# Kernel optimization log

Measured on AMD Instinct MI355X. Metric: run time of the kernel, lower is better.

## Reference

```python
import jax, jax.numpy as jnp
import numpy as np

V = 100000   # vertices
C = 64       # in channels
D = 64       # out channels
W = 8        # weight matrices
DEG = 16     # neighbors per vertex
E = V * DEG  # edges


def setup_inputs() -> dict:
    key = jax.random.key(0)
    k = jax.random.split(key, 6)
    data = jax.random.normal(k[0], (V, C), dtype=jnp.float32)
    # fixed-degree adjacency: vertex i has DEG neighbors (arbitrary dst)
    edge_src = jnp.repeat(jnp.arange(V, dtype=jnp.int32), DEG)        # [E] sorted
    edge_dst = jax.random.randint(k[1], (E,), 0, V, dtype=jnp.int32)  # [E]
    edge_vals = jnp.full((E,), 1.0 / DEG, dtype=jnp.float32)          # row-normalized
    var_u = 0.1 * jax.random.normal(k[2], (C, W), dtype=jnp.float32)
    var_c = 0.1 * jax.random.normal(k[3], (W,), dtype=jnp.float32)
    var_w = 0.1 * jax.random.normal(k[4], (W, C, D), dtype=jnp.float32)
    var_b = 0.1 * jax.random.normal(k[5], (D,), dtype=jnp.float32)
    return {"data": data, "edge_src": edge_src, "edge_dst": edge_dst,
            "edge_vals": edge_vals, "var_u": var_u, "var_c": var_c,
            "var_w": var_w, "var_b": var_b}


def reference(data, edge_src, edge_dst, edge_vals, var_u, var_c, var_w, var_b):
    # translation_invariant=True => var_v = -var_u
    num_v = data.shape[0]
    x_u = data @ var_u            # [V, W]
    x_v = data @ (-var_u)         # [V, W]
    # edge logits and exp-normalize over the W weight matrices (softmax == exp/sum)
    logits = x_u[edge_src] + x_v[edge_dst] + var_c   # [E, W]
    q = jax.nn.softmax(logits, axis=-1)              # [E, W]
    # gathered neighbor features, pre-scaled by adjacency values
    x_sep = data[edge_dst] * edge_vals[:, None]      # [E, C]
    y = jnp.zeros((num_v, var_w.shape[-1]), dtype=data.dtype)
    for m in range(var_c.shape[0]):  # small fixed loop over W weight matrices
        agg = jax.ops.segment_sum(q[:, m:m + 1] * x_sep, edge_src,
                                  num_segments=num_v)  # [V, C]
        y = y + agg @ var_w[m]                          # [V, D]
    return y + var_b
```

## Files before the change

### kernel.cpp

```cpp
#include <hip/hip_runtime.h>

typedef _Float16 half2_t __attribute__((ext_vector_type(2)));
typedef _Float16 half4_t __attribute__((ext_vector_type(4)));
typedef _Float16 half8_t __attribute__((ext_vector_type(8)));
typedef __attribute__((ext_vector_type(4))) float f32x4;

#define NV 100000
#define NTILE 6250
#define GRID 512
#define LDSZ 81920

#define VMWAIT(N) asm volatile("s_waitcnt vmcnt(" #N ")" ::: "memory")
#define LGKM0     asm volatile("s_waitcnt lgkmcnt(0)" ::: "memory")
#define FENCE     asm volatile("" ::: "memory")

__device__ __forceinline__ unsigned cvt_pk_u(float a, float b) {
  auto h = __builtin_amdgcn_cvt_pkrtz(a, b);
  return __builtin_bit_cast(unsigned, h);
}
__device__ __forceinline__ half2_t u2h(unsigned u) { return __builtin_bit_cast(half2_t, u); }
__device__ __forceinline__ unsigned lds_off(const void* p) {
  return (unsigned)(size_t)(const __attribute__((address_space(3))) char*)p;
}
__device__ __forceinline__ void load16_to_lds(const void* g, void* s) {
  __builtin_amdgcn_global_load_lds(
      (const __attribute__((address_space(1))) unsigned int*)g,
      (__attribute__((address_space(3))) unsigned int*)s, 16, 0, 0);
}

__global__ __launch_bounds__(256) void k1_prep(const float* __restrict__ data,
                                               const float* __restrict__ var_u,
                                               const float* __restrict__ var_w,
                                               unsigned short* __restrict__ data_h,
                                               unsigned short* __restrict__ xu_h,
                                               unsigned short* __restrict__ Bt) {
  __shared__ float u_lds[512];
  int tid = threadIdx.x;
  if (blockIdx.x < 128) {
    int t = blockIdx.x * 256 + tid;
    int d = t >> 9, k = t & 511;
    _Float16 h = (_Float16)var_w[k * 64 + d];
    Bt[t] = __builtin_bit_cast(unsigned short, h);
  }
  u_lds[tid] = var_u[tid];
  u_lds[tid + 256] = var_u[tid + 256];
  __syncthreads();
  int v = blockIdx.x * 256 + tid;
  if (v >= NV) return;
  const float4* dp = (const float4*)(data + v * 64);
  float acc[8];
#pragma unroll
  for (int w = 0; w < 8; ++w) acc[w] = 0.f;
  uint4* ob = (uint4*)(data_h + v * 64);
#pragma unroll
  for (int q = 0; q < 8; ++q) {
    float4 a4 = dp[q * 2], b4 = dp[q * 2 + 1];
    int c0 = q * 8;
#pragma unroll
    for (int w = 0; w < 8; ++w)
      acc[w] += a4.x * u_lds[(c0 + 0) * 8 + w] + a4.y * u_lds[(c0 + 1) * 8 + w]
              + a4.z * u_lds[(c0 + 2) * 8 + w] + a4.w * u_lds[(c0 + 3) * 8 + w]
              + b4.x * u_lds[(c0 + 4) * 8 + w] + b4.y * u_lds[(c0 + 5) * 8 + w]
              + b4.z * u_lds[(c0 + 6) * 8 + w] + b4.w * u_lds[(c0 + 7) * 8 + w];
    uint4 pk;
    pk.x = cvt_pk_u(a4.x, a4.y); pk.y = cvt_pk_u(a4.z, a4.w);
    pk.z = cvt_pk_u(b4.x, b4.y); pk.w = cvt_pk_u(b4.z, b4.w);
    ob[q] = pk;
  }
  uint4 xp;
  xp.x = cvt_pk_u(acc[0], acc[1]); xp.y = cvt_pk_u(acc[2], acc[3]);
  xp.z = cvt_pk_u(acc[4], acc[5]); xp.w = cvt_pk_u(acc[6], acc[7]);
  *(uint4*)(xu_h + v * 8) = xp;
}

#define PREPASS(XUDs, LINs, XS)                                               \
  {                                                                           \
    uint4 xd4 = *(const uint4*)((XUDs) + (wave * 64 + l) * 16);               \
    float evv = ((const float*)((LINs) + 1024))[wave * 64 + l];               \
    half2_t xm01 = u2h((XS).x), xm23 = u2h((XS).y);                           \
    half2_t xm45 = u2h((XS).z), xm67 = u2h((XS).w);                           \
    half2_t xd01 = u2h(xd4.x), xd23 = u2h(xd4.y);                             \
    half2_t xd45 = u2h(xd4.z), xd67 = u2h(xd4.w);                             \
    float ex0 = __expf((float)xm01[0] - (float)xd01[0] + c8[0]);              \
    float ex1 = __expf((float)xm01[1] - (float)xd01[1] + c8[1]);              \
    float ex2 = __expf((float)xm23[0] - (float)xd23[0] + c8[2]);              \
    float ex3 = __expf((float)xm23[1] - (float)xd23[1] + c8[3]);              \
    float ex4 = __expf((float)xm45[0] - (float)xd45[0] + c8[4]);              \
    float ex5 = __expf((float)xm45[1] - (float)xd45[1] + c8[5]);              \
    float ex6 = __expf((float)xm67[0] - (float)xd67[0] + c8[6]);              \
    float ex7 = __expf((float)xm67[1] - (float)xd67[1] + c8[7]);              \
    float ssum = ((ex0 + ex1) + (ex2 + ex3)) + ((ex4 + ex5) + (ex6 + ex7));   \
    float rs = __builtin_amdgcn_rcpf(ssum) * evv;                             \
    uint4 qq;                                                                 \
    qq.x = cvt_pk_u(ex0 * rs, ex1 * rs);                                      \
    qq.y = cvt_pk_u(ex2 * rs, ex3 * rs);                                      \
    qq.z = cvt_pk_u(ex4 * rs, ex5 * rs);                                      \
    qq.w = cvt_pk_u(ex6 * rs, ex7 * rs);                                      \
    int vv = l >> 4, jq = (l >> 2) & 3, jl = l & 3;                           \
    char* qb = (XUDs) + wave * 1024 + vv * 256;                               \
    _Pragma("unroll")                                                         \
    for (int m = 0; m < 8; ++m) {                                             \
      unsigned short hv = (unsigned short)((&qq.x)[m >> 1] >> ((m & 1) * 16));\
      int byte = (((m ^ vv) & 7) << 5) + (((jq ^ vv ^ m) & 3) << 3) + jl * 2; \
      *(unsigned short*)(qb + byte) = hv;                                     \
    }                                                                         \
  }

__global__ __launch_bounds__(256, 2) void k2_main(
    const unsigned short* __restrict__ data_h,
    const unsigned short* __restrict__ xu_h,
    const int* __restrict__ edge_dst,
    const float* __restrict__ edge_vals,
    const unsigned short* __restrict__ Bt,
    const float* __restrict__ var_c,
    const float* __restrict__ var_b,
    float* __restrict__ y) {
  extern __shared__ __align__(16) char smem[];
  char* XB0  = smem;
  char* XUD0 = smem + 65536;
  char* LIN0 = smem + 73728;

  int tid = threadIdx.x;
  int wave = tid >> 6;
  int l = tid & 63;
  int q4 = l >> 4;
  int row = l & 15;
  int col = row + wave * 16;

  uint4 btf[16];
#pragma unroll
  for (int ks = 0; ks < 16; ++ks)
    btf[ks] = *(const uint4*)(Bt + (col * 512 + ks * 32 + q4 * 8));
  float c8[8];
#pragma unroll
  for (int m = 0; m < 8; ++m) c8[m] = var_c[m];
  float bias = var_b[col];

#define LIN_DMA(SL, TS)                                                        \
  { char* lb_ = LIN0 + (SL) * 2048;                                            \
    if ((wave & 1) == 0)                                                       \
      load16_to_lds(edge_dst + (size_t)(TS) * 256 + l * 4, lb_);               \
    else                                                                       \
      load16_to_lds(edge_vals + (size_t)(TS) * 256 + l * 4, lb_ + 1024); }
#define XUD_DMA(SL, LSL)                                                       \
  { const int* ld_ = (const int*)(LIN0 + (LSL) * 2048);                        \
    int dv_ = ld_[wave * 64 + l];                                              \
    load16_to_lds(xu_h + (size_t)dv_ * 8, XUD0 + (SL) * 4096 + wave * 1024); }
#define X_DMA(SL, LSL)                                                         \
  { const int* ld_ = (const int*)(LIN0 + (LSL) * 2048);                        \
    int j_ = ((l >> 3) & 3) * 4 + ((l >> 1) & 3);                              \
    int ch0_ = ((l >> 5) << 1) | (l & 1);                                      \
    _Pragma("unroll")                                                          \
    for (int s_ = 0; s_ < 8; ++s_) {                                           \
      int dv_ = ld_[wave * 64 + (s_ >> 1) * 16 + j_];                          \
      int ch_ = ch0_ + (s_ & 1) * 4;                                           \
      load16_to_lds(data_h + (size_t)dv_ * 64 + ch_ * 8,                       \
                    XB0 + (SL) * 32768 + wave * 8192 + s_ * 1024); } }

  int t0 = blockIdx.x;
  int tG1 = (t0 + GRID < NTILE) ? t0 + GRID : t0;
  int tG2 = (t0 + 2 * GRID < NTILE) ? t0 + 2 * GRID : t0;
  FENCE;
  LIN_DMA(0, t0);
  LIN_DMA(1, tG1);
  LIN_DMA(2, tG2);
  FENCE;
  uint4 xsA = *(const uint4*)(xu_h + ((size_t)t0 * 16 + wave * 4 + q4) * 8);
  uint4 xsB = *(const uint4*)(xu_h + ((size_t)tG1 * 16 + wave * 4 + q4) * 8);
  VMWAIT(0);
  __builtin_amdgcn_s_barrier();
  FENCE;
  XUD_DMA(0, 0);
  X_DMA(0, 0);
  FENCE;
  VMWAIT(0);
  __builtin_amdgcn_s_barrier();
  PREPASS(XUD0, LIN0, xsA);
  LGKM0;

  int kc = 0;
  for (int t = t0; t < NTILE; t += GRID, ++kc) {
    int slc = kc & 1, lslc = kc & 3;
    int sl1 = (kc + 1) & 1, lsl1 = (kc + 1) & 3, lsl3 = (kc + 3) & 3;
    int t2c = (t + 2 * GRID < NTILE) ? t + 2 * GRID : t;
    int t3c = (t + 3 * GRID < NTILE) ? t + 3 * GRID : t;
    char* XBt = XB0 + slc * 32768;
    char* XUDt = XUD0 + slc * 4096;
    char* XUDn = XUD0 + sl1 * 4096;
    const char* LINn = LIN0 + lsl1 * 2048;
    (void)lslc;

    FENCE;
    XUD_DMA(sl1, lsl1);
    X_DMA(sl1, lsl1);
    FENCE;

    {
      uint2 qfr[4];
#pragma unroll
      for (int vv = 0; vv < 4; ++vv) {
        int srow = (row ^ vv) & 7;
        int gsl = (q4 ^ vv ^ row) & 3;
        qfr[vv] = *(const uint2*)(XUDt + wave * 1024 + vv * 256 + srow * 32 + gsl * 8);
      }
      unsigned xbase = lds_off(XBt + wave * 8192) + l * 8;
      uint2 trd[16];
#pragma unroll
      for (int vv = 0; vv < 4; ++vv)
#pragma unroll
        for (int cb = 0; cb < 4; ++cb) {
          unsigned a_ = xbase + vv * 2048 + cb * 512;
          asm volatile("ds_read_b64_tr_b16 %0, %1"
                       : "=v"(trd[vv * 4 + cb]) : "v"(a_) : "memory");
        }
      LGKM0;
      __builtin_amdgcn_sched_barrier(0);
      f32x4 D[16];
      __builtin_amdgcn_s_setprio(1);
#pragma unroll
      for (int vv = 0; vv < 4; ++vv)
#pragma unroll
        for (int cb = 0; cb < 4; ++cb) {
          f32x4 z = {0.f, 0.f, 0.f, 0.f};
          D[vv * 4 + cb] = __builtin_amdgcn_mfma_f32_16x16x16f16(
              __builtin_bit_cast(half4_t, trd[vv * 4 + cb]),
              __builtin_bit_cast(half4_t, qfr[vv]), z, 0, 0, 0);
        }
      __builtin_amdgcn_s_setprio(0);
      if (row < 8) {
#pragma unroll
        for (int vv = 0; vv < 4; ++vv) {
          int vg = wave * 4 + vv;
          char* ab = XBt + vg * 2048;
#pragma unroll
          for (int cb = 0; cb < 4; ++cb) {
            f32x4 d4 = D[vv * 4 + cb];
            uint2 w2;
            w2.x = cvt_pk_u(d4[0], d4[1]);
            w2.y = cvt_pk_u(d4[2], d4[3]);
            int byte = (row * 128 + cb * 32 + q4 * 8) ^ ((vg & 7) << 4)
                       ^ ((row & 3) << 5);
            *(uint2*)(ab + byte) = w2;
          }
        }
      }
    }

    VMWAIT(8);
    PREPASS(XUDn, LINn, xsB);

    FENCE;
    uint4 xsC = *(const uint4*)(xu_h + ((size_t)t2c * 16 + wave * 4 + q4) * 8);
    FENCE;
    LIN_DMA(lsl3, t3c);
    FENCE;

    LGKM0;
    __builtin_amdgcn_s_barrier();

    {
      f32x4 C0 = {0.f, 0.f, 0.f, 0.f};
      f32x4 C1 = {0.f, 0.f, 0.f, 0.f};
      __builtin_amdgcn_s_setprio(1);
#pragma unroll
      for (int ks2 = 0; ks2 < 8; ++ks2) {
        int ka = 2 * ks2, kb = 2 * ks2 + 1;
        int boa = (ka * 64 + q4 * 16) ^ ((row & 7) << 4) ^ (((ka >> 1) & 3) << 5);
        int bob = (kb * 64 + q4 * 16) ^ ((row & 7) << 4) ^ (((kb >> 1) & 3) << 5);
        half8_t afa = *(const half8_t*)(XBt + row * 2048 + boa);
        half8_t afb = *(const half8_t*)(XBt + row * 2048 + bob);
        C0 = __builtin_amdgcn_mfma_f32_16x16x32_f16(
            afa, __builtin_bit_cast(half8_t, btf[ka]), C0, 0, 0, 0);
        C1 = __builtin_amdgcn_mfma_f32_16x16x32_f16(
            afb, __builtin_bit_cast(half8_t, btf[kb]), C1, 0, 0, 0);
      }
      __builtin_amdgcn_s_setprio(0);
#pragma unroll
      for (int i = 0; i < 4; ++i)
        y[(size_t)(t * 16 + q4 * 4 + i) * 64 + col] = C0[i] + C1[i] + bias;
    }
    LGKM0;
    VMWAIT(4);
    __builtin_amdgcn_s_barrier();

    xsB = xsC;
    (void)xsA;
  }
  VMWAIT(0);
#undef LIN_DMA
#undef XUD_DMA
#undef X_DMA
}

extern "C" void kernel_launch(void* const* d_in, const int* in_sizes, int n_in,
                              void* d_out, int out_size, void* d_ws, size_t ws_size,
                              hipStream_t stream) {
  const float* data      = (const float*)d_in[0];
  const int*   edge_dst  = (const int*)d_in[2];
  const float* edge_vals = (const float*)d_in[3];
  const float* var_u     = (const float*)d_in[4];
  const float* var_c     = (const float*)d_in[5];
  const float* var_w     = (const float*)d_in[6];
  const float* var_b     = (const float*)d_in[7];
  float* y = (float*)d_out;

  char* ws = (char*)d_ws;
  unsigned short* data_h = (unsigned short*)ws;
  unsigned short* xu_h   = (unsigned short*)(ws + 12800000);
  unsigned short* Bt     = (unsigned short*)(ws + 14400000);

  hipFuncSetAttribute((const void*)k2_main,
                      hipFuncAttributeMaxDynamicSharedMemorySize, LDSZ);

  hipLaunchKernelGGL(k1_prep, dim3((NV + 255) / 256), dim3(256), 0, stream,
                     data, var_u, var_w, data_h, xu_h, Bt);
  hipLaunchKernelGGL(k2_main, dim3(GRID), dim3(256), LDSZ, stream,
                     data_h, xu_h, edge_dst, edge_vals, Bt, var_c, var_b, y);
}
```

Measured before the change: 67.18 us.

## Fuse prep kernel into main kernel with a global atomic grid barrier

The fp16 conversion of data, the x·u projection and the var_w transpose now run at the start of the persistent main kernel instead of in a separate prep launch. A global atomic counter, cleared by a memset beforehand, acts as a grid-wide barrier so that all 512 blocks finish the prep writes before the tiled gather and MFMA phase reads them. The aim is to remove the gap between the two kernels. The barrier only works if all 512 blocks are resident at once, and the memset is still an extra operation on the stream.

```diff
diff --git a/kernel.cpp b/kernel.cpp
--- a/kernel.cpp
+++ b/kernel.cpp
@@ -26,51 +26,6 @@
   __builtin_amdgcn_global_load_lds(
       (const __attribute__((address_space(1))) unsigned int*)g,
       (__attribute__((address_space(3))) unsigned int*)s, 16, 0, 0);
-}
-
-__global__ __launch_bounds__(256) void k1_prep(const float* __restrict__ data,
-                                               const float* __restrict__ var_u,
-                                               const float* __restrict__ var_w,
-                                               unsigned short* __restrict__ data_h,
-                                               unsigned short* __restrict__ xu_h,
-                                               unsigned short* __restrict__ Bt) {
-  __shared__ float u_lds[512];
-  int tid = threadIdx.x;
-  if (blockIdx.x < 128) {
-    int t = blockIdx.x * 256 + tid;
-    int d = t >> 9, k = t & 511;
-    _Float16 h = (_Float16)var_w[k * 64 + d];
-    Bt[t] = __builtin_bit_cast(unsigned short, h);
-  }
-  u_lds[tid] = var_u[tid];
-  u_lds[tid + 256] = var_u[tid + 256];
-  __syncthreads();
-  int v = blockIdx.x * 256 + tid;
-  if (v >= NV) return;
-  const float4* dp = (const float4*)(data + v * 64);
-  float acc[8];
-#pragma unroll
-  for (int w = 0; w < 8; ++w) acc[w] = 0.f;
-  uint4* ob = (uint4*)(data_h + v * 64);
-#pragma unroll
-  for (int q = 0; q < 8; ++q) {
-    float4 a4 = dp[q * 2], b4 = dp[q * 2 + 1];
-    int c0 = q * 8;
-#pragma unroll
-    for (int w = 0; w < 8; ++w)
-      acc[w] += a4.x * u_lds[(c0 + 0) * 8 + w] + a4.y * u_lds[(c0 + 1) * 8 + w]
-              + a4.z * u_lds[(c0 + 2) * 8 + w] + a4.w * u_lds[(c0 + 3) * 8 + w]
-              + b4.x * u_lds[(c0 + 4) * 8 + w] + b4.y * u_lds[(c0 + 5) * 8 + w]
-              + b4.z * u_lds[(c0 + 6) * 8 + w] + b4.w * u_lds[(c0 + 7) * 8 + w];
-    uint4 pk;
-    pk.x = cvt_pk_u(a4.x, a4.y); pk.y = cvt_pk_u(a4.z, a4.w);
-    pk.z = cvt_pk_u(b4.x, b4.y); pk.w = cvt_pk_u(b4.z, b4.w);
-    ob[q] = pk;
-  }
-  uint4 xp;
-  xp.x = cvt_pk_u(acc[0], acc[1]); xp.y = cvt_pk_u(acc[2], acc[3]);
-  xp.z = cvt_pk_u(acc[4], acc[5]); xp.w = cvt_pk_u(acc[6], acc[7]);
-  *(uint4*)(xu_h + v * 8) = xp;
 }
 
 #define PREPASS(XUDs, LINs, XS)                                               \
@@ -106,14 +61,18 @@
     }                                                                         \
   }
 
-__global__ __launch_bounds__(256, 2) void k2_main(
-    const unsigned short* __restrict__ data_h,
-    const unsigned short* __restrict__ xu_h,
+__global__ __launch_bounds__(256, 2) void k2_fused(
+    const float* __restrict__ data,
+    const float* __restrict__ var_u,
+    const float* __restrict__ var_w,
     const int* __restrict__ edge_dst,
     const float* __restrict__ edge_vals,
-    const unsigned short* __restrict__ Bt,
     const float* __restrict__ var_c,
     const float* __restrict__ var_b,
+    unsigned short* __restrict__ data_h,
+    unsigned short* __restrict__ xu_h,
+    unsigned short* __restrict__ Bt,
+    unsigned* __restrict__ gsync,
     float* __restrict__ y) {
   extern __shared__ __align__(16) char smem[];
   char* XB0  = smem;
@@ -121,6 +80,57 @@
   char* LIN0 = smem + 73728;
 
   int tid = threadIdx.x;
+
+  {
+    float* u_lds = (float*)smem;
+    if (blockIdx.x < 128) {
+      int t = blockIdx.x * 256 + tid;
+      int d = t >> 9, k = t & 511;
+      _Float16 h = (_Float16)var_w[k * 64 + d];
+      Bt[t] = __builtin_bit_cast(unsigned short, h);
+    }
+    u_lds[tid] = var_u[tid];
+    u_lds[tid + 256] = var_u[tid + 256];
+    __syncthreads();
+    int v = blockIdx.x * 256 + tid;
+    if (v < NV) {
+      const float4* dp = (const float4*)(data + v * 64);
+      float acc[8];
+#pragma unroll
+      for (int w = 0; w < 8; ++w) acc[w] = 0.f;
+      uint4* ob = (uint4*)(data_h + v * 64);
+#pragma unroll
+      for (int q = 0; q < 8; ++q) {
+        float4 a4 = dp[q * 2], b4 = dp[q * 2 + 1];
+        int c0 = q * 8;
+#pragma unroll
+        for (int w = 0; w < 8; ++w)
+          acc[w] += a4.x * u_lds[(c0 + 0) * 8 + w] + a4.y * u_lds[(c0 + 1) * 8 + w]
+                  + a4.z * u_lds[(c0 + 2) * 8 + w] + a4.w * u_lds[(c0 + 3) * 8 + w]
+                  + b4.x * u_lds[(c0 + 4) * 8 + w] + b4.y * u_lds[(c0 + 5) * 8 + w]
+                  + b4.z * u_lds[(c0 + 6) * 8 + w] + b4.w * u_lds[(c0 + 7) * 8 + w];
+        uint4 pk;
+        pk.x = cvt_pk_u(a4.x, a4.y); pk.y = cvt_pk_u(a4.z, a4.w);
+        pk.z = cvt_pk_u(b4.x, b4.y); pk.w = cvt_pk_u(b4.z, b4.w);
+        ob[q] = pk;
+      }
+      uint4 xp;
+      xp.x = cvt_pk_u(acc[0], acc[1]); xp.y = cvt_pk_u(acc[2], acc[3]);
+      xp.z = cvt_pk_u(acc[4], acc[5]); xp.w = cvt_pk_u(acc[6], acc[7]);
+      *(uint4*)(xu_h + v * 8) = xp;
+    }
+  }
+  __threadfence();
+  __syncthreads();
+  if (tid == 0) {
+    __hip_atomic_fetch_add(gsync, 1u, __ATOMIC_RELEASE, __HIP_MEMORY_SCOPE_AGENT);
+    while (__hip_atomic_load(gsync, __ATOMIC_ACQUIRE, __HIP_MEMORY_SCOPE_AGENT)
+           < (unsigned)GRID)
+      __builtin_amdgcn_s_sleep(8);
+  }
+  __syncthreads();
+  __threadfence();
+
   int wave = tid >> 6;
   int l = tid & 63;
   int q4 = l >> 4;
@@ -180,7 +190,7 @@
 
   int kc = 0;
   for (int t = t0; t < NTILE; t += GRID, ++kc) {
-    int slc = kc & 1, lslc = kc & 3;
+    int slc = kc & 1;
     int sl1 = (kc + 1) & 1, lsl1 = (kc + 1) & 3, lsl3 = (kc + 3) & 3;
     int t2c = (t + 2 * GRID < NTILE) ? t + 2 * GRID : t;
     int t3c = (t + 3 * GRID < NTILE) ? t + 3 * GRID : t;
@@ -188,7 +198,6 @@
     char* XUDt = XUD0 + slc * 4096;
     char* XUDn = XUD0 + sl1 * 4096;
     const char* LINn = LIN0 + lsl1 * 2048;
-    (void)lslc;
 
     FENCE;
     XUD_DMA(sl1, lsl1);
@@ -308,12 +317,13 @@
   unsigned short* data_h = (unsigned short*)ws;
   unsigned short* xu_h   = (unsigned short*)(ws + 12800000);
   unsigned short* Bt     = (unsigned short*)(ws + 14400000);
-
-  hipFuncSetAttribute((const void*)k2_main,
+  unsigned*       gsync  = (unsigned*)(ws + 14465536);
+
+  hipFuncSetAttribute((const void*)k2_fused,
                       hipFuncAttributeMaxDynamicSharedMemorySize, LDSZ);
 
-  hipLaunchKernelGGL(k1_prep, dim3((NV + 255) / 256), dim3(256), 0, stream,
-                     data, var_u, var_w, data_h, xu_h, Bt);
-  hipLaunchKernelGGL(k2_main, dim3(GRID), dim3(256), LDSZ, stream,
-                     data_h, xu_h, edge_dst, edge_vals, Bt, var_c, var_b, y);
-}
+  hipMemsetAsync((void*)gsync, 0, 4, stream);
+  hipLaunchKernelGGL(k2_fused, dim3(GRID), dim3(256), LDSZ, stream,
+                     data, var_u, var_w, edge_dst, edge_vals, var_c, var_b,
+                     data_h, xu_h, Bt, gsync, y);
+}
```

After: 257.8 us. 284% more time.

## Coalesce prep kernel loads with 16 lanes per vertex and shuffle reduction

Applied to the files above, without the earlier changes.

The prep kernel previously had each thread read a full 256-byte vertex row, so global loads were strided and uncoalesced. It now assigns 16 lanes per vertex, each loading one float4, and computes the 8 projections with partial dot products followed by a xor-shuffle reduction. var_u is transposed in LDS to match the new access pattern. This buys coalesced loads and stores at the cost of extra shuffle instructions, and only lane 0 of each group writes xu_h. The unused lslc variable in the main kernel is also removed.

```diff
diff --git a/kernel.cpp b/kernel.cpp
--- a/kernel.cpp
+++ b/kernel.cpp
@@ -42,35 +42,43 @@
     _Float16 h = (_Float16)var_w[k * 64 + d];
     Bt[t] = __builtin_bit_cast(unsigned short, h);
   }
-  u_lds[tid] = var_u[tid];
-  u_lds[tid + 256] = var_u[tid + 256];
+  u_lds[(tid & 7) * 64 + (tid >> 3)] = var_u[tid];
+  {
+    int e2 = tid + 256;
+    u_lds[(e2 & 7) * 64 + (e2 >> 3)] = var_u[e2];
+  }
   __syncthreads();
-  int v = blockIdx.x * 256 + tid;
-  if (v >= NV) return;
-  const float4* dp = (const float4*)(data + v * 64);
-  float acc[8];
-#pragma unroll
-  for (int w = 0; w < 8; ++w) acc[w] = 0.f;
-  uint4* ob = (uint4*)(data_h + v * 64);
-#pragma unroll
-  for (int q = 0; q < 8; ++q) {
-    float4 a4 = dp[q * 2], b4 = dp[q * 2 + 1];
-    int c0 = q * 8;
+  int wave = tid >> 6, l = tid & 63;
+  int vb = blockIdx.x * 256 + wave * 64;
+  int vsub = l >> 4;
+  int c4 = l & 15;
+#pragma unroll 4
+  for (int it = 0; it < 16; ++it) {
+    int v = vb + it * 4 + vsub;
+    float4 d4 = {0.f, 0.f, 0.f, 0.f};
+    if (v < NV) d4 = *(const float4*)(data + (size_t)v * 64 + c4 * 4);
+    float acc[8];
 #pragma unroll
     for (int w = 0; w < 8; ++w)
-      acc[w] += a4.x * u_lds[(c0 + 0) * 8 + w] + a4.y * u_lds[(c0 + 1) * 8 + w]
-              + a4.z * u_lds[(c0 + 2) * 8 + w] + a4.w * u_lds[(c0 + 3) * 8 + w]
-              + b4.x * u_lds[(c0 + 4) * 8 + w] + b4.y * u_lds[(c0 + 5) * 8 + w]
-              + b4.z * u_lds[(c0 + 6) * 8 + w] + b4.w * u_lds[(c0 + 7) * 8 + w];
-    uint4 pk;
-    pk.x = cvt_pk_u(a4.x, a4.y); pk.y = cvt_pk_u(a4.z, a4.w);
-    pk.z = cvt_pk_u(b4.x, b4.y); pk.w = cvt_pk_u(b4.z, b4.w);
-    ob[q] = pk;
-  }
-  uint4 xp;
-  xp.x = cvt_pk_u(acc[0], acc[1]); xp.y = cvt_pk_u(acc[2], acc[3]);
-  xp.z = cvt_pk_u(acc[4], acc[5]); xp.w = cvt_pk_u(acc[6], acc[7]);
-  *(uint4*)(xu_h + v * 8) = xp;
+      acc[w] = d4.x * u_lds[w * 64 + c4 * 4 + 0] + d4.y * u_lds[w * 64 + c4 * 4 + 1]
+             + d4.z * u_lds[w * 64 + c4 * 4 + 2] + d4.w * u_lds[w * 64 + c4 * 4 + 3];
+#pragma unroll
+    for (int mk = 1; mk < 16; mk <<= 1)
+#pragma unroll
+      for (int w = 0; w < 8; ++w) acc[w] += __shfl_xor(acc[w], mk);
+    if (v < NV) {
+      uint2 pk;
+      pk.x = cvt_pk_u(d4.x, d4.y);
+      pk.y = cvt_pk_u(d4.z, d4.w);
+      *(uint2*)(data_h + (size_t)v * 64 + c4 * 4) = pk;
+      if (c4 == 0) {
+        uint4 xp;
+        xp.x = cvt_pk_u(acc[0], acc[1]); xp.y = cvt_pk_u(acc[2], acc[3]);
+        xp.z = cvt_pk_u(acc[4], acc[5]); xp.w = cvt_pk_u(acc[6], acc[7]);
+        *(uint4*)(xu_h + (size_t)v * 8) = xp;
+      }
+    }
+  }
 }
 
 #define PREPASS(XUDs, LINs, XS)                                               \
@@ -180,7 +188,7 @@
 
   int kc = 0;
   for (int t = t0; t < NTILE; t += GRID, ++kc) {
-    int slc = kc & 1, lslc = kc & 3;
+    int slc = kc & 1;
     int sl1 = (kc + 1) & 1, lsl1 = (kc + 1) & 3, lsl3 = (kc + 3) & 3;
     int t2c = (t + 2 * GRID < NTILE) ? t + 2 * GRID : t;
     int t3c = (t + 3 * GRID < NTILE) ? t + 3 * GRID : t;
@@ -188,7 +196,6 @@
     char* XUDt = XUD0 + slc * 4096;
     char* XUDn = XUD0 + sl1 * 4096;
     const char* LINn = LIN0 + lsl1 * 2048;
-    (void)lslc;
 
     FENCE;
     XUD_DMA(sl1, lsl1);
```

Measured after the change: 71.07 us. 5.8% more time.
